# Kernel tuning notes

Measured on AMD Instinct MI355X. Metric: run time of the kernel, lower is better.

The kernel has to match this reference:

```python
import jax, jax.numpy as jnp
from jax import lax
import numpy as np

N, K, F, H, NG, T = 32768, 16, 64, 128, 1024, 2


def setup_inputs() -> dict:
    key = jax.random.key(0)
    ks = jax.random.split(key, 24)
    def rn(k, shape, s=0.05):
        return jax.random.normal(k, shape, jnp.float32) * s
    inp = {
        'n': jax.random.normal(ks[0], (N, F), jnp.float32),
        'nbr': jax.random.randint(ks[1], (N, K), 0, N),
        # deterministic sorted graph ids -> every graph non-empty (safe segment_max)
        'gid': (jnp.arange(N) * NG) // N,
        'G': NG,
        # SAGEConv layer 1: LSTM(F,F), fc_self/fc_neigh F->H
        'lstm1_Wih': rn(ks[2], (F, 4 * F)), 'lstm1_Whh': rn(ks[3], (F, 4 * F)), 'lstm1_b': jnp.zeros((4 * F,), jnp.float32),
        'fcs1_W': rn(ks[4], (F, H)), 'fcs1_b': jnp.zeros((H,), jnp.float32),
        'fcn1_W': rn(ks[5], (F, H)), 'fcn1_b': jnp.zeros((H,), jnp.float32),
        # SAGEConv layer 2: LSTM(H,H), fc_self/fc_neigh H->H
        'lstm2_Wih': rn(ks[6], (H, 4 * H)), 'lstm2_Whh': rn(ks[7], (H, 4 * H)), 'lstm2_b': jnp.zeros((4 * H,), jnp.float32),
        'fcs2_W': rn(ks[8], (H, H)), 'fcs2_b': jnp.zeros((H,), jnp.float32),
        'fcn2_W': rn(ks[9], (H, H)), 'fcn2_b': jnp.zeros((H,), jnp.float32),
        # WeightedSumAndMax atom weighting: H->1
        'rw_W': rn(ks[10], (H, 1)), 'rw_b': jnp.zeros((1,), jnp.float32),
        # task head: 2H->H, H->T
        'h1_W': rn(ks[11], (2 * H, H)), 'h1_b': jnp.zeros((H,), jnp.float32),
        'h2_W': rn(ks[12], (H, T)), 'h2_b': jnp.zeros((T,), jnp.float32),
    }
    return inp


def _lstm_last(xseq, Wih, Whh, b):
    # xseq: [N, K, Fin]; returns last hidden state [N, Hh]
    Hh = Whh.shape[0]
    h0 = jnp.zeros((xseq.shape[0], Hh), xseq.dtype)
    def step(carry, xt):
        h, c = carry
        g = xt @ Wih + h @ Whh + b  # [N, 4H], torch gate order i,f,g,o
        i, f, gg, o = jnp.split(g, 4, axis=-1)
        c = jax.nn.sigmoid(f) * c + jax.nn.sigmoid(i) * jnp.tanh(gg)
        h = jax.nn.sigmoid(o) * jnp.tanh(c)
        return (h, c), None
    (h, _), _ = lax.scan(step, (h0, h0), jnp.swapaxes(xseq, 0, 1))
    return h


def _sage_layer(x, nbr, Wih, Whh, b, Ws, bs, Wn, bn):
    hn = _lstm_last(x[nbr], Wih, Whh, b)          # LSTM aggregate of neighbors
    return jax.nn.sigmoid(x @ Ws + bs + hn @ Wn + bn)


def reference(n, nbr, gid, G,
              lstm1_Wih, lstm1_Whh, lstm1_b, fcs1_W, fcs1_b, fcn1_W, fcn1_b,
              lstm2_Wih, lstm2_Whh, lstm2_b, fcs2_W, fcs2_b, fcn2_W, fcn2_b,
              rw_W, rw_b, h1_W, h1_b, h2_W, h2_b):
    G = int(G)
    h1 = _sage_layer(n, nbr, lstm1_Wih, lstm1_Whh, lstm1_b, fcs1_W, fcs1_b, fcn1_W, fcn1_b)
    h2 = _sage_layer(h1, nbr, lstm2_Wih, lstm2_Whh, lstm2_b, fcs2_W, fcs2_b, fcn2_W, fcn2_b)
    # WeightedSumAndMax readout
    w = jax.nn.sigmoid(h2 @ rw_W + rw_b)                       # [N,1]
    wsum = jax.ops.segment_sum(w * h2, gid, num_segments=G)    # [G,H]
    mx = jax.ops.segment_max(h2, gid, num_segments=G)          # [G,H]
    gemb = jnp.concatenate([wsum, mx], axis=-1)                # [G,2H]
    y = jax.nn.sigmoid(gemb @ h1_W + h1_b)
    y = jax.nn.sigmoid(y @ h2_W + h2_b)                        # classification
    return y
```

## Files before the change

### kernel.cpp

```cpp
#include <hip/hip_runtime.h>

typedef unsigned short u16;
typedef __attribute__((ext_vector_type(8))) short bf16x8;
typedef __attribute__((ext_vector_type(4))) float f32x4;
typedef __attribute__((ext_vector_type(2))) float f32x2;

constexpr int N_ = 32768;
constexpr int H_ = 128;
constexpr int G_ = 1024;
constexpr int T_ = 2;

__device__ __forceinline__ float sigf(float x){
  float e = __builtin_amdgcn_exp2f(x * -1.44269504f);
  return __builtin_amdgcn_rcpf(1.0f + e);
}
__device__ __forceinline__ f32x2 sig2(f32x2 x){
  f32x2 t = x * -1.44269504f;
  f32x2 e; e.x = __builtin_amdgcn_exp2f(t.x); e.y = __builtin_amdgcn_exp2f(t.y);
  f32x2 d = e + 1.0f;
  float r = __builtin_amdgcn_rcpf(d.x * d.y);
  return (f32x2){r * d.y, r * d.x};
}
__device__ __forceinline__ f32x2 tanh2(f32x2 x){
  f32x2 t = x * 2.88539008f;
  f32x2 e; e.x = __builtin_amdgcn_exp2f(t.x); e.y = __builtin_amdgcn_exp2f(t.y);
  f32x2 d = e + 1.0f;
  float r = __builtin_amdgcn_rcpf(d.x * d.y);
  f32x2 rr = (f32x2){r * d.y, r * d.x};
  return 1.0f - 2.0f*rr;
}
__device__ __forceinline__ u16 f2bf(float f){
  unsigned u = __float_as_uint(f);
  unsigned r = (u + 0x7FFFu + ((u>>16)&1u))>>16;
  return (u16)r;
}
__device__ __forceinline__ unsigned cvt_pk_bf16(float a, float b){
  unsigned r;
  asm("v_cvt_pk_bf16_f32 %0, %1, %2" : "=v"(r) : "v"(a), "v"(b));
  return r;
}
__device__ __forceinline__ float bf2f(u16 h){ return __uint_as_float(((unsigned)h)<<16); }
__device__ __forceinline__ float asf(unsigned u){ return __uint_as_float(u); }
__device__ __forceinline__ f32x4 mfma16(bf16x8 a, bf16x8 b, f32x4 c){
  return __builtin_amdgcn_mfma_f32_16x16x32_bf16(a,b,c,0,0,0);
}

__global__ __launch_bounds__(64)
void pack_all(const float* __restrict__ l1Wih, const float* __restrict__ fcs1W,
              const float* __restrict__ l1Whh, const float* __restrict__ fcn1W,
              const float* __restrict__ l2Wih, const float* __restrict__ fcs2W,
              const float* __restrict__ l2Whh, const float* __restrict__ fcn2W,
              const float* __restrict__ l1b, const float* __restrict__ bs1,
              const float* __restrict__ bn1,
              const float* __restrict__ l2b, const float* __restrict__ bs2,
              const float* __restrict__ bn2,
              u16* BY1, u16* BW1, u16* BN1, u16* BY2, u16* BW2, u16* BN2,
              u16* bY1, u16* bY2)
{
  int b = blockIdx.x;
  const int lane = threadIdx.x;
  if (b == 416) {
    for (int i = lane; i < 1024; i += 64) {
      if (i < 384) {
        int p = i; float v;
        if (p < 256) { int o = (p&3)*64 + ((p>>6)<<4) + ((p>>2)&15); v = l1b[o]; }
        else         { int j = p-256; v = bs1[j] + bn1[j]; }
        bY1[p] = f2bf(v);
      } else {
        int p = i - 384; float v;
        if (p < 512) { int o = (p&3)*128 + ((p>>6)<<4) + ((p>>2)&15); v = l2b[o]; }
        else         { int j = p-512; v = bs2[j] + bn2[j]; }
        bY2[p] = f2bf(v);
      }
    }
    return;
  }
  const float* src; u16* dst; int srcNC, NTtot, ntOff, ntCnt, Fh, perm;
  if      (b < 32)  { src=l1Wih; dst=BY1; srcNC=256; NTtot=24; ntOff=0;  ntCnt=16; Fh=64;  perm=2; }
  else if (b < 48)  { src=fcs1W; dst=BY1; srcNC=128; NTtot=24; ntOff=16; ntCnt=8;  Fh=0;   perm=0; b-=32; }
  else if (b < 80)  { src=l1Whh; dst=BW1; srcNC=256; NTtot=16; ntOff=0;  ntCnt=16; Fh=64;  perm=1; b-=48; }
  else if (b < 96)  { src=fcn1W; dst=BN1; srcNC=128; NTtot=8;  ntOff=0;  ntCnt=8;  Fh=0;   perm=0; b-=80; }
  else if (b < 224) { src=l2Wih; dst=BY2; srcNC=512; NTtot=40; ntOff=0;  ntCnt=32; Fh=128; perm=2; b-=96; }
  else if (b < 256) { src=fcs2W; dst=BY2; srcNC=128; NTtot=40; ntOff=32; ntCnt=8;  Fh=0;   perm=0; b-=224; }
  else if (b < 384) { src=l2Whh; dst=BW2; srcNC=512; NTtot=32; ntOff=0;  ntCnt=32; Fh=128; perm=1; b-=256; }
  else              { src=fcn2W; dst=BN2; srcNC=128; NTtot=8;  ntOff=0;  ntCnt=8;  Fh=0;   perm=0; b-=384; }
  const int ntl = b % ntCnt, kt = b / ntCnt;
  const int n = lane & 15, qq = lane >> 4;
  int pr = ntl*16 + n;
  int o;
  if (perm == 1)      o = ((pr>>4)&3)*Fh + ((pr>>6)<<4) + (pr&15);
  else if (perm == 2) o = (pr&3)*Fh + ((pr>>6)<<4) + ((pr>>2)&15);
  else                o = pr;
  u16* d = dst + ((size_t)((kt*NTtot + ntOff + ntl)*64 + lane))*8;
#pragma unroll
  for (int j = 0; j < 8; ++j) {
    int k = kt*32 + qq*8 + j;
    d[j] = f2bf(src[(size_t)k*srcNC + o]);
  }
}

template<int KT, int NTT, int AF32>
__global__ __launch_bounds__(256, 2)
void gemm_kernel(const void* __restrict__ Ain,
                 const u16* __restrict__ Bpk,
                 const u16* __restrict__ biasbf,
                 u16* __restrict__ out, int out_stride)
{
  constexpr int KA  = KT*32;
  constexpr int NTW = NTT/4;
  constexpr int STR = KA + 8;
  __shared__ __align__(16) u16 a_lds[32*STR];
  const int tid  = threadIdx.x;
  const int base = blockIdx.x*32;
  {
    const int sub = tid & 7, rowl = tid >> 3;
    if constexpr (AF32) {
      const float* src = (const float*)Ain + (size_t)(base+rowl)*KA;
#pragma unroll
      for (int cc = 0; cc < KA/32; ++cc) {
        int e0 = (cc*8+sub)*4;
        float4 v = *(const float4*)(src + e0);
        ushort4 bv;
        bv.x = f2bf(v.x); bv.y = f2bf(v.y); bv.z = f2bf(v.z); bv.w = f2bf(v.w);
        *(ushort4*)(void*)(a_lds + rowl*STR + e0) = bv;
      }
    } else {
      const u16* src = (const u16*)Ain + (size_t)(base+rowl)*KA;
#pragma unroll
      for (int cc = 0; cc < KA/64; ++cc) {
        int e0 = (cc*8+sub)*8;
        uint4 v = *(const uint4*)(const void*)(src + e0);
        *(uint4*)(void*)(a_lds + rowl*STR + e0) = v;
      }
    }
  }
  __syncthreads();
  const int lane = tid & 63, w = tid >> 6;
  const int lc = lane & 15, q = lane >> 4;
  f32x4 acc[2][NTW];
  f32x4 z = {0.f,0.f,0.f,0.f};
#pragma unroll
  for (int m = 0; m < 2; ++m)
#pragma unroll
    for (int j = 0; j < NTW; ++j) acc[m][j] = z;
#pragma unroll
  for (int kt = 0; kt < KT; ++kt) {
    bf16x8 af0 = *(const bf16x8*)(const void*)(a_lds + lc*STR      + kt*32 + q*8);
    bf16x8 af1 = *(const bf16x8*)(const void*)(a_lds + (lc+16)*STR + kt*32 + q*8);
#pragma unroll
    for (int j = 0; j < NTW; ++j) {
      bf16x8 bf = *(const bf16x8*)(const void*)(Bpk + ((size_t)((kt*NTT + w*NTW + j)*64 + lane))*8);
      acc[0][j] = mfma16(af0, bf, acc[0][j]);
      acc[1][j] = mfma16(af1, bf, acc[1][j]);
    }
  }
#pragma unroll
  for (int m = 0; m < 2; ++m)
#pragma unroll
    for (int j = 0; j < NTW; ++j) {
      int col = (w*NTW + j)*16 + lc;
#pragma unroll
      for (int r = 0; r < 4; ++r) {
        int row = base + m*16 + q*4 + r;
        out[(size_t)row*out_stride + col] = f2bf(acc[m][j][r] + bf2f(biasbf[col]));
      }
    }
}

template<int KT, int MT, int MW>
__global__ __launch_bounds__(KT*128, MW)
void lstm_kernel(const int* __restrict__ nbr,
                 const u16* __restrict__ Y, int nctot,
                 const u16* __restrict__ Bpk,
                 const u16* __restrict__ BN,
                 const u16* __restrict__ Sp, int s_stride, int s_coloff,
                 u16* __restrict__ out)
{
  constexpr int F   = KT*32;
  constexpr int NW  = KT*2;
  constexpr int NTT = KT*8;
  constexpr int STR = F + 8;
  constexpr int M   = MT*16;
  __shared__ __align__(16) u16 h_lds[2][M*STR];
  __shared__ int nbr_s[M*16];
  const int tid  = threadIdx.x;
  const int base = blockIdx.x * M;
  const int lane = tid & 63, w = tid >> 6;
  const int lc = lane & 15, q = lane >> 4;

  for (int i = tid; i < M*16; i += NW*64) nbr_s[i] = nbr[base*16 + i];

  bf16x8 bfr[KT][4];
#pragma unroll
  for (int kt = 0; kt < KT; ++kt)
#pragma unroll
    for (int g = 0; g < 4; ++g)
      bfr[kt][g] = *(const bf16x8*)(const void*)(Bpk + ((size_t)((kt*NTT + w*4 + g)*64 + lane))*8);

  f32x2 cs[MT][2];
#pragma unroll
  for (int m = 0; m < MT; ++m)
#pragma unroll
    for (int rp = 0; rp < 2; ++rp) cs[m][rp] = (f32x2){0.f, 0.f};
  __syncthreads();

  const char* Yb = (const char*)Y;
  const unsigned rowbytes = (unsigned)nctot * 2u;
  const unsigned lanebyte = (unsigned)(w*64 + lc*4) * 2u;
  const int wcol = w*16 + lc;

  uint2 yv[MT][4];
#pragma unroll
  for (int m = 0; m < MT; ++m)
#pragma unroll
    for (int r = 0; r < 4; ++r) {
      unsigned vr = (unsigned)nbr_s[(m*16 + q*4 + r)*16];
      yv[m][r] = *(const uint2*)(const void*)(Yb + (vr*rowbytes + lanebyte));
    }

  for (int t = 0; t < 16; ++t) {
    const u16* hr = h_lds[t & 1];
    u16*       hw = h_lds[(t & 1) ^ 1];
#pragma unroll
    for (int m = 0; m < MT; ++m) {
      f32x4 acc[4];
      f32x4 z = {0.f,0.f,0.f,0.f};
#pragma unroll
      for (int g = 0; g < 4; ++g) acc[g] = z;
      if (t != 0) {
#pragma unroll
        for (int kt = 0; kt < KT; ++kt) {
          bf16x8 af = *(const bf16x8*)(const void*)(hr + (lc + m*16)*STR + kt*32 + q*8);
#pragma unroll
          for (int g = 0; g < 4; ++g) acc[g] = mfma16(af, bfr[kt][g], acc[g]);
        }
      }
#pragma unroll
      for (int rp = 0; rp < 2; ++rp) {
        uint2 ya = yv[m][2*rp], yb = yv[m][2*rp+1];
        f32x2 yi = { asf(ya.x<<16),          asf(yb.x<<16) };
        f32x2 yf = { asf(ya.x&0xffff0000u),  asf(yb.x&0xffff0000u) };
        f32x2 yg = { asf(ya.y<<16),          asf(yb.y<<16) };
        f32x2 yo = { asf(ya.y&0xffff0000u),  asf(yb.y&0xffff0000u) };
        f32x2 gi = (f32x2){acc[0][2*rp], acc[0][2*rp+1]} + yi;
        f32x2 gf = (f32x2){acc[1][2*rp], acc[1][2*rp+1]} + yf;
        f32x2 gg = (f32x2){acc[2][2*rp], acc[2][2*rp+1]} + yg;
        f32x2 go = (f32x2){acc[3][2*rp], acc[3][2*rp+1]} + yo;
        f32x2 c  = sig2(gf)*cs[m][rp] + sig2(gi)*tanh2(gg);
        cs[m][rp] = c;
        f32x2 hh = sig2(go)*tanh2(c);
        unsigned pkd = cvt_pk_bf16(hh.x, hh.y);
        int r0 = m*16 + q*4 + 2*rp;
        hw[r0*STR + wcol]     = (u16)pkd;
        hw[(r0+1)*STR + wcol] = (u16)(pkd >> 16);
      }
    }
    if (t < 15) {
#pragma unroll
      for (int m = 0; m < MT; ++m)
#pragma unroll
        for (int r = 0; r < 4; ++r) {
          unsigned vr = (unsigned)nbr_s[(m*16 + q*4 + r)*16 + t + 1];
          yv[m][r] = *(const uint2*)(const void*)(Yb + (vr*rowbytes + lanebyte));
        }
    }
    __syncthreads();
  }

  constexpr int CPW = 8 / NW;
  const u16* hf = h_lds[0];
#pragma unroll
  for (int cc2 = 0; cc2 < CPW; ++cc2) {
    const int nt = w*CPW + cc2;
    f32x4 a2[MT];
    f32x4 z = {0.f,0.f,0.f,0.f};
#pragma unroll
    for (int m = 0; m < MT; ++m) a2[m] = z;
#pragma unroll
    for (int kt = 0; kt < KT; ++kt) {
      bf16x8 nf = *(const bf16x8*)(const void*)(BN + ((size_t)((kt*8 + nt)*64 + lane))*8);
#pragma unroll
      for (int m = 0; m < MT; ++m) {
        bf16x8 af = *(const bf16x8*)(const void*)(hf + (lc + m*16)*STR + kt*32 + q*8);
        a2[m] = mfma16(af, nf, a2[m]);
      }
    }
    const int col = nt*16 + lc;
#pragma unroll
    for (int m = 0; m < MT; ++m)
#pragma unroll
      for (int r = 0; r < 4; ++r) {
        int row = base + m*16 + q*4 + r;
        float v = a2[m][r] + bf2f(Sp[(size_t)row*s_stride + s_coloff + col]);
        out[(size_t)row*H_ + col] = f2bf(sigf(v));
      }
  }
}

__global__ __launch_bounds__(128)
void head_kernel(const u16* __restrict__ h2, const float* __restrict__ rwW,
                 const float* __restrict__ rwb,
                 const float* __restrict__ h1W, const float* __restrict__ h1b,
                 const float* __restrict__ h2W, const float* __restrict__ h2b,
                 float* __restrict__ out)
{
  __shared__ float h2s[32*H_];
  __shared__ float part[32*4];
  __shared__ float wv[32];
  __shared__ float gemb[2*H_];
  __shared__ float y1[H_];
  const int g = blockIdx.x, t = threadIdx.x;
  for (int r = 0; r < 32; ++r)
    h2s[r*H_ + t] = bf2f(h2[(size_t)(g*32 + r)*H_ + t]);
  __syncthreads();
  { int r = t>>2, qq = t&3; float p = 0.f;
    for (int h = qq*32; h < qq*32+32; ++h) p += h2s[r*H_+h]*rwW[h];
    part[r*4+qq] = p; }
  __syncthreads();
  if (t < 32) wv[t] = sigf(part[t*4]+part[t*4+1]+part[t*4+2]+part[t*4+3]+rwb[0]);
  __syncthreads();
  { float wsum=0.f, mx=-3.402823466e38f;
    for (int r = 0; r < 32; ++r) { float v = h2s[r*H_+t]; wsum += wv[r]*v; mx = fmaxf(mx,v); }
    gemb[t]=wsum; gemb[H_+t]=mx; }
  __syncthreads();
  { float a = h1b[t];
    for (int k = 0; k < 2*H_; ++k) a += gemb[k]*h1W[k*H_+t];
    y1[t]=sigf(a); }
  __syncthreads();
  if (t < T_) {
    float a = h2b[t];
    for (int h = 0; h < H_; ++h) a += y1[h]*h2W[h*T_+t];
    out[(size_t)g*T_+t] = sigf(a);
  }
}

extern "C" void kernel_launch(void* const* d_in, const int* in_sizes, int n_in,
                              void* d_out, int out_size, void* d_ws, size_t ws_size,
                              hipStream_t stream) {
  const float* n_feat = (const float*)d_in[0];
  const int*   nbr    = (const int*)d_in[1];
  const float* l1Wih = (const float*)d_in[4];
  const float* l1Whh = (const float*)d_in[5];
  const float* l1b   = (const float*)d_in[6];
  const float* fcs1W = (const float*)d_in[7];
  const float* fcs1b = (const float*)d_in[8];
  const float* fcn1W = (const float*)d_in[9];
  const float* fcn1b = (const float*)d_in[10];
  const float* l2Wih = (const float*)d_in[11];
  const float* l2Whh = (const float*)d_in[12];
  const float* l2b   = (const float*)d_in[13];
  const float* fcs2W = (const float*)d_in[14];
  const float* fcs2b = (const float*)d_in[15];
  const float* fcn2W = (const float*)d_in[16];
  const float* fcn2b = (const float*)d_in[17];
  const float* rwW   = (const float*)d_in[18];
  const float* rwb   = (const float*)d_in[19];
  const float* h1W   = (const float*)d_in[20];
  const float* h1b   = (const float*)d_in[21];
  const float* h2W   = (const float*)d_in[22];
  const float* h2b   = (const float*)d_in[23];

  char* ws = (char*)d_ws;
  u16* Y   = (u16*)(ws);
  u16* h1  = (u16*)(ws + 41943040);
  u16* h2  = (u16*)(ws + 50331648);
  char* wt = ws + 58720256;
  u16* BY1 = (u16*)(wt);
  u16* BW1 = (u16*)(wt + 49152);
  u16* BN1 = (u16*)(wt + 81920);
  u16* BY2 = (u16*)(wt + 98304);
  u16* BW2 = (u16*)(wt + 262144);
  u16* BN2 = (u16*)(wt + 393216);
  u16* bY1 = (u16*)(wt + 425984);
  u16* bY2 = (u16*)(wt + 426752);

  pack_all<<<417, 64, 0, stream>>>(l1Wih, fcs1W, l1Whh, fcn1W,
                                   l2Wih, fcs2W, l2Whh, fcn2W,
                                   l1b, fcs1b, fcn1b, l2b, fcs2b, fcn2b,
                                   BY1, BW1, BN1, BY2, BW2, BN2, bY1, bY2);

  gemm_kernel<2,24,1><<<1024, 256, 0, stream>>>(n_feat, BY1, bY1, Y, 384);
  lstm_kernel<2,1,6><<<2048, 256, 0, stream>>>(nbr, Y, 384, BW1, BN1, Y, 384, 256, h1);

  gemm_kernel<4,40,0><<<1024, 256, 0, stream>>>(h1, BY2, bY2, Y, 640);
  lstm_kernel<4,1,4><<<2048, 512, 0, stream>>>(nbr, Y, 640, BW2, BN2, Y, 640, 512, h2);

  head_kernel<<<G_, 128, 0, stream>>>(h2, rwW, rwb, h1W, h1b, h2W, h2b, (float*)d_out);
}
```

Before: 301.8 us.

## Fuse layer-1 input projection into LSTM kernel, gathering raw bf16 features

```diff
diff --git a/kernel.cpp b/kernel.cpp
--- a/kernel.cpp
+++ b/kernel.cpp
@@ -54,18 +54,21 @@
               const float* __restrict__ bn1,
               const float* __restrict__ l2b, const float* __restrict__ bs2,
               const float* __restrict__ bn2,
-              u16* BY1, u16* BW1, u16* BN1, u16* BY2, u16* BW2, u16* BN2,
-              u16* bY1, u16* bY2)
+              u16* BI1, u16* BW1, u16* BS1, u16* BN1,
+              u16* BY2, u16* BW2, u16* BN2,
+              u16* bG1, u16* bsn1, u16* bY2)
 {
   int b = blockIdx.x;
   const int lane = threadIdx.x;
   if (b == 416) {
     for (int i = lane; i < 1024; i += 64) {
-      if (i < 384) {
-        int p = i; float v;
-        if (p < 256) { int o = (p&3)*64 + ((p>>6)<<4) + ((p>>2)&15); v = l1b[o]; }
-        else         { int j = p-256; v = bs1[j] + bn1[j]; }
-        bY1[p] = f2bf(v);
+      if (i < 256) {
+        int p = i;
+        int o = ((p>>4)&3)*64 + ((p>>6)<<4) + (p&15);
+        bG1[p] = f2bf(l1b[o]);
+      } else if (i < 384) {
+        int j = i - 256;
+        bsn1[j] = f2bf(bs1[j] + bn1[j]);
       } else {
         int p = i - 384; float v;
         if (p < 512) { int o = (p&3)*128 + ((p>>6)<<4) + ((p>>2)&15); v = l2b[o]; }
@@ -76,9 +79,9 @@
     return;
   }
   const float* src; u16* dst; int srcNC, NTtot, ntOff, ntCnt, Fh, perm;
-  if      (b < 32)  { src=l1Wih; dst=BY1; srcNC=256; NTtot=24; ntOff=0;  ntCnt=16; Fh=64;  perm=2; }
-  else if (b < 48)  { src=fcs1W; dst=BY1; srcNC=128; NTtot=24; ntOff=16; ntCnt=8;  Fh=0;   perm=0; b-=32; }
-  else if (b < 80)  { src=l1Whh; dst=BW1; srcNC=256; NTtot=16; ntOff=0;  ntCnt=16; Fh=64;  perm=1; b-=48; }
+  if      (b < 32)  { src=l1Wih; dst=BI1; srcNC=256; NTtot=16; ntOff=0;  ntCnt=16; Fh=64;  perm=1; }
+  else if (b < 64)  { src=l1Whh; dst=BW1; srcNC=256; NTtot=16; ntOff=0;  ntCnt=16; Fh=64;  perm=1; b-=32; }
+  else if (b < 80)  { src=fcs1W; dst=BS1; srcNC=128; NTtot=8;  ntOff=0;  ntCnt=8;  Fh=0;   perm=0; b-=64; }
   else if (b < 96)  { src=fcn1W; dst=BN1; srcNC=128; NTtot=8;  ntOff=0;  ntCnt=8;  Fh=0;   perm=0; b-=80; }
   else if (b < 224) { src=l2Wih; dst=BY2; srcNC=512; NTtot=40; ntOff=0;  ntCnt=32; Fh=128; perm=2; b-=96; }
   else if (b < 256) { src=fcs2W; dst=BY2; srcNC=128; NTtot=40; ntOff=32; ntCnt=8;  Fh=0;   perm=0; b-=224; }
@@ -96,6 +99,139 @@
   for (int j = 0; j < 8; ++j) {
     int k = kt*32 + qq*8 + j;
     d[j] = f2bf(src[(size_t)k*srcNC + o]);
+  }
+}
+
+__global__ __launch_bounds__(256)
+void cast_kernel(const float* __restrict__ X, u16* __restrict__ Xbf)
+{
+  int i = (blockIdx.x*256 + threadIdx.x)*8;
+  float4 a = *(const float4*)(X + i);
+  float4 b = *(const float4*)(X + i + 4);
+  ushort4 r0, r1;
+  r0.x=f2bf(a.x); r0.y=f2bf(a.y); r0.z=f2bf(a.z); r0.w=f2bf(a.w);
+  r1.x=f2bf(b.x); r1.y=f2bf(b.y); r1.z=f2bf(b.z); r1.w=f2bf(b.w);
+  *(ushort4*)(void*)(Xbf + i)     = r0;
+  *(ushort4*)(void*)(Xbf + i + 4) = r1;
+}
+
+__global__ __launch_bounds__(256, 4)
+void lstm1_fused(const int* __restrict__ nbr, const u16* __restrict__ Xbf,
+                 const u16* __restrict__ BI, const u16* __restrict__ BW,
+                 const u16* __restrict__ BS, const u16* __restrict__ BNw,
+                 const u16* __restrict__ bG, const u16* __restrict__ bsn,
+                 u16* __restrict__ out)
+{
+  constexpr int STR = 72;
+  __shared__ __align__(16) u16 h_lds[2][16*STR];
+  __shared__ __align__(16) u16 x_lds[2][16*STR];
+  __shared__ int nbr_s[256];
+  const int tid  = threadIdx.x;
+  const int base = blockIdx.x * 16;
+  const int lane = tid & 63, w = tid >> 6;
+  const int lc = lane & 15, q = lane >> 4;
+
+  nbr_s[tid] = nbr[base*16 + tid];
+
+  bf16x8 bw[2][4], bx[2][4];
+#pragma unroll
+  for (int kt = 0; kt < 2; ++kt)
+#pragma unroll
+    for (int g = 0; g < 4; ++g) {
+      bw[kt][g] = *(const bf16x8*)(const void*)(BW + ((size_t)((kt*16 + w*4 + g)*64 + lane))*8);
+      bx[kt][g] = *(const bf16x8*)(const void*)(BI + ((size_t)((kt*16 + w*4 + g)*64 + lane))*8);
+    }
+  float b4[4];
+#pragma unroll
+  for (int g = 0; g < 4; ++g) b4[g] = bf2f(bG[w*64 + g*16 + lc]);
+
+  f32x2 cs[2];
+  cs[0] = (f32x2){0.f,0.f}; cs[1] = (f32x2){0.f,0.f};
+
+  const int srow = tid >> 4, scol = tid & 15;
+  __syncthreads();
+  {
+    unsigned vr = (unsigned)nbr_s[srow*16 + 0];
+    uint2 v = *(const uint2*)(const void*)((const char*)Xbf + (vr*128u + scol*8u));
+    *(uint2*)(void*)((char*)&x_lds[0][0] + srow*144 + scol*8) = v;
+  }
+  __syncthreads();
+
+  const int wcol = w*16 + lc;
+  for (int t = 0; t < 16; ++t) {
+    const u16* hr = h_lds[t & 1];
+    const u16* xr = x_lds[t & 1];
+    u16*       hw = h_lds[(t & 1) ^ 1];
+    uint2 pv;
+    if (t < 15) {
+      unsigned vr = (unsigned)nbr_s[srow*16 + t + 1];
+      pv = *(const uint2*)(const void*)((const char*)Xbf + (vr*128u + scol*8u));
+    }
+    f32x4 acc[4];
+#pragma unroll
+    for (int g = 0; g < 4; ++g)
+#pragma unroll
+      for (int r = 0; r < 4; ++r) acc[g][r] = b4[g];
+#pragma unroll
+    for (int kt = 0; kt < 2; ++kt) {
+      bf16x8 af = *(const bf16x8*)(const void*)(xr + lc*STR + kt*32 + q*8);
+#pragma unroll
+      for (int g = 0; g < 4; ++g) acc[g] = mfma16(af, bx[kt][g], acc[g]);
+    }
+    if (t != 0) {
+#pragma unroll
+      for (int kt = 0; kt < 2; ++kt) {
+        bf16x8 af = *(const bf16x8*)(const void*)(hr + lc*STR + kt*32 + q*8);
+#pragma unroll
+        for (int g = 0; g < 4; ++g) acc[g] = mfma16(af, bw[kt][g], acc[g]);
+      }
+    }
+#pragma unroll
+    for (int rp = 0; rp < 2; ++rp) {
+      f32x2 gi = (f32x2){acc[0][2*rp], acc[0][2*rp+1]};
+      f32x2 gf = (f32x2){acc[1][2*rp], acc[1][2*rp+1]};
+      f32x2 gg = (f32x2){acc[2][2*rp], acc[2][2*rp+1]};
+      f32x2 go = (f32x2){acc[3][2*rp], acc[3][2*rp+1]};
+      f32x2 c  = sig2(gf)*cs[rp] + sig2(gi)*tanh2(gg);
+      cs[rp] = c;
+      f32x2 hh = sig2(go)*tanh2(c);
+      unsigned pkd = cvt_pk_bf16(hh.x, hh.y);
+      int r0 = q*4 + 2*rp;
+      hw[r0*STR + wcol]     = (u16)pkd;
+      hw[(r0+1)*STR + wcol] = (u16)(pkd >> 16);
+    }
+    if (t < 15)
+      *(uint2*)(void*)((char*)&x_lds[(t & 1) ^ 1][0] + srow*144 + scol*8) = pv;
+    __syncthreads();
+  }
+
+  {
+    uint2 v = *(const uint2*)(const void*)((const char*)Xbf + ((unsigned)(base + srow)*128u + scol*8u));
+    *(uint2*)(void*)((char*)&x_lds[0][0] + srow*144 + scol*8) = v;
+  }
+  __syncthreads();
+  const u16* hf = h_lds[0];
+  const u16* xf = x_lds[0];
+#pragma unroll
+  for (int cc = 0; cc < 2; ++cc) {
+    const int nt = w*2 + cc;
+    const int col = nt*16 + lc;
+    f32x4 a2;
+    float bv = bf2f(bsn[col]);
+#pragma unroll
+    for (int r = 0; r < 4; ++r) a2[r] = bv;
+#pragma unroll
+    for (int kt = 0; kt < 2; ++kt) {
+      bf16x8 sf = *(const bf16x8*)(const void*)(BS  + ((size_t)((kt*8 + nt)*64 + lane))*8);
+      bf16x8 nf = *(const bf16x8*)(const void*)(BNw + ((size_t)((kt*8 + nt)*64 + lane))*8);
+      bf16x8 ax = *(const bf16x8*)(const void*)(xf + lc*STR + kt*32 + q*8);
+      bf16x8 ah = *(const bf16x8*)(const void*)(hf + lc*STR + kt*32 + q*8);
+      a2 = mfma16(ax, sf, a2);
+      a2 = mfma16(ah, nf, a2);
+    }
+#pragma unroll
+    for (int r = 0; r < 4; ++r)
+      out[(size_t)(base + q*4 + r)*H_ + col] = f2bf(sigf(a2[r]));
   }
 }
 
@@ -362,25 +498,29 @@
 
   char* ws = (char*)d_ws;
   u16* Y   = (u16*)(ws);
-  u16* h1  = (u16*)(ws + 41943040);
-  u16* h2  = (u16*)(ws + 50331648);
-  char* wt = ws + 58720256;
-  u16* BY1 = (u16*)(wt);
-  u16* BW1 = (u16*)(wt + 49152);
-  u16* BN1 = (u16*)(wt + 81920);
-  u16* BY2 = (u16*)(wt + 98304);
-  u16* BW2 = (u16*)(wt + 262144);
-  u16* BN2 = (u16*)(wt + 393216);
-  u16* bY1 = (u16*)(wt + 425984);
-  u16* bY2 = (u16*)(wt + 426752);
+  u16* Xbf = (u16*)(ws + 41943040);
+  u16* h1  = (u16*)(ws + 46137344);
+  u16* h2  = (u16*)(ws + 54525952);
+  char* wt = ws + 62914560;
+  u16* BI1  = (u16*)(wt);
+  u16* BW1  = (u16*)(wt + 32768);
+  u16* BS1  = (u16*)(wt + 65536);
+  u16* BN1  = (u16*)(wt + 81920);
+  u16* BY2  = (u16*)(wt + 98304);
+  u16* BW2  = (u16*)(wt + 262144);
+  u16* BN2  = (u16*)(wt + 393216);
+  u16* bG1  = (u16*)(wt + 425984);
+  u16* bsn1 = (u16*)(wt + 426496);
+  u16* bY2  = (u16*)(wt + 426752);
 
   pack_all<<<417, 64, 0, stream>>>(l1Wih, fcs1W, l1Whh, fcn1W,
                                    l2Wih, fcs2W, l2Whh, fcn2W,
                                    l1b, fcs1b, fcn1b, l2b, fcs2b, fcn2b,
-                                   BY1, BW1, BN1, BY2, BW2, BN2, bY1, bY2);
-
-  gemm_kernel<2,24,1><<<1024, 256, 0, stream>>>(n_feat, BY1, bY1, Y, 384);
-  lstm_kernel<2,1,6><<<2048, 256, 0, stream>>>(nbr, Y, 384, BW1, BN1, Y, 384, 256, h1);
+                                   BI1, BW1, BS1, BN1, BY2, BW2, BN2,
+                                   bG1, bsn1, bY2);
+
+  cast_kernel<<<1024, 256, 0, stream>>>(n_feat, Xbf);
+  lstm1_fused<<<2048, 256, 0, stream>>>(nbr, Xbf, BI1, BW1, BS1, BN1, bG1, bsn1, h1);
 
   gemm_kernel<4,40,0><<<1024, 256, 0, stream>>>(h1, BY2, bY2, Y, 640);
   lstm_kernel<4,1,4><<<2048, 512, 0, stream>>>(nbr, Y, 640, BW2, BN2, Y, 640, 512, h2);
```

New measurement: 305.6 us. Within noise of the previous version (+1.3%).
